# Kernel tuning notes

Measured on AMD Instinct MI355X. Metric: run time of the kernel, lower is better.

The kernel has to match this reference:

```python
import jax, jax.numpy as jnp
import numpy as np

B, N, M = 256, 512, 512


def setup_inputs() -> dict:
    key = jax.random.key(0)
    kx, kw, kt = jax.random.split(key, 3)
    x = jax.random.uniform(kx, (B, N), dtype=jnp.float32)
    w = jax.random.uniform(kw, (N, M), dtype=jnp.float32)
    t = jax.random.uniform(kt, (B, M), dtype=jnp.float32)
    return {"x": x, "w": w, "t": t}


def reference(x, w, t):
    # x: [B, N], w: [N, M], t: [B, M]
    x3 = x[:, :, None]   # [B, N, 1]
    t3 = t[:, None, :]   # [B, 1, M]
    w3 = w[None, :, :]   # [1, N, M]

    # relevance of x per (n, m): sum over batch of min(x, t) / sum over batch of x
    rel_x = jnp.minimum(x3, t3).sum(axis=0, keepdims=True) / x3.sum(axis=0, keepdims=True)  # [1, N, M]
    # relevance of w per (b, m): sum over N of min(w, t) / sum over N of w
    rel_w = jnp.minimum(w3, t3).sum(axis=-2, keepdims=True) / w3.sum(axis=-2, keepdims=True)  # [B, 1, M]

    # argmax over the N (inner) dimension
    ind_w = jnp.argmax(jnp.minimum(x3, rel_x), axis=-2)  # [B, M]
    ind_x = jnp.argmax(jnp.minimum(rel_w, w3), axis=-2)  # [B, M]

    # inner_x and inner_w are numerically identical in forward (detach only affects grads)
    inner = jnp.minimum(x3, w3)  # [B, N, M]
    chosen_x = jnp.take_along_axis(inner, ind_x[:, None, :], axis=-2)[:, 0, :]  # [B, M]
    chosen_w = jnp.take_along_axis(inner, ind_w[:, None, :], axis=-2)[:, 0, :]  # [B, M]
    return (chosen_x, chosen_w)
```

## Files before the change

kernel.cpp:

```cpp
#include <hip/hip_runtime.h>

#define B 256
#define N 512
#define M 512
#define BM (B * M)


__device__ __forceinline__ void tile_tr256(const float* __restrict__ src,
                                           float* __restrict__ dst,
                                           int R, int C, int r0, int c0, int tid) {
    __shared__ float s[64][65];
    const int tx = tid & 63, q = tid >> 6;
    #pragma unroll
    for (int j = 0; j < 16; ++j) {
        int rl = q * 16 + j;
        s[rl][tx] = src[(r0 + rl) * C + c0 + tx];
    }
    __syncthreads();
    #pragma unroll
    for (int j = 0; j < 16; ++j) {
        int cl = q * 16 + j;
        dst[(c0 + cl) * R + r0 + tx] = s[tx][cl];
    }
}

__global__ __launch_bounds__(256) void k_a(const float* __restrict__ x,
                                           const float* __restrict__ w,
                                           const float* __restrict__ t,
                                           float* __restrict__ xT,
                                           float* __restrict__ wT,
                                           float* __restrict__ tT,
                                           float* __restrict__ rvp) {
    const int blk = blockIdx.x, tid = threadIdx.x;
    if (blk < 128) {
        const int m0 = (blk & 7) * 64;
        const int n0 = (blk >> 3) * 32;
        const int tx = tid & 15, ty = tid >> 4;
        __shared__ float  s_t[32][64];
        __shared__ float  s_x[32][36];
        __shared__ double sxc4[32][4];
        const int sr = tid >> 3, sc = tid & 7;
        const int nA = ty * 2, nB = nA + 1;
        float pA0, pA1, pA2, pA3, pB0, pB1, pB2, pB3;
        #pragma unroll
        for (int z = 0; z < 4; ++z) {
            float aA0 = 0.f, aA1 = 0.f, aA2 = 0.f, aA3 = 0.f;
            float aB0 = 0.f, aB1 = 0.f, aB2 = 0.f, aB3 = 0.f;
            for (int scnk = 0; scnk < 2; ++scnk) {
                const int bb = z * 64 + scnk * 32;
                __syncthreads();
                *(float4*)&s_t[sr][sc * 8]     = *(const float4*)&t[(bb + sr) * M + m0 + sc * 8];
                *(float4*)&s_t[sr][sc * 8 + 4] = *(const float4*)&t[(bb + sr) * M + m0 + sc * 8 + 4];
                *(float4*)&s_x[sr][sc * 4]     = *(const float4*)&x[(bb + sr) * N + n0 + sc * 4];
                __syncthreads();
                #pragma unroll 8
                for (int i = 0; i < 32; ++i) {
                    float4 tv = *(const float4*)&s_t[i][tx * 4];
                    float xA = s_x[i][nA], xB = s_x[i][nB];
                    aA0 += fminf(xA, tv.x); aA1 += fminf(xA, tv.y);
                    aA2 += fminf(xA, tv.z); aA3 += fminf(xA, tv.w);
                    aB0 += fminf(xB, tv.x); aB1 += fminf(xB, tv.y);
                    aB2 += fminf(xB, tv.z); aB3 += fminf(xB, tv.w);
                }
            }
            if (z == 0) {
                pA0 = aA0; pA1 = aA1; pA2 = aA2; pA3 = aA3;
                pB0 = aB0; pB1 = aB1; pB2 = aB2; pB3 = aB3;
            } else {
                pA0 += aA0; pA1 += aA1; pA2 += aA2; pA3 += aA3;
                pB0 += aB0; pB1 += aB1; pB2 += aB2; pB3 += aB3;
            }
        }
        if (tid < 128) {
            const int col = n0 + (tid >> 2), ch = tid & 3;
            double a = 0.0;
            for (int b = ch; b < B; b += 4) a += (double)x[b * N + col];
            sxc4[tid >> 2][ch] = a;
        }
        __syncthreads();
        const float sA = (float)((sxc4[nA][0] + sxc4[nA][1]) + (sxc4[nA][2] + sxc4[nA][3]));
        const float sB = (float)((sxc4[nB][0] + sxc4[nB][1]) + (sxc4[nB][2] + sxc4[nB][3]));
        float* so = &s_t[0][0];
        so[(tx * 4 + 0) * 32 + nA] = pA0 / sA; so[(tx * 4 + 0) * 32 + nB] = pB0 / sB;
        so[(tx * 4 + 1) * 32 + nA] = pA1 / sA; so[(tx * 4 + 1) * 32 + nB] = pB1 / sB;
        so[(tx * 4 + 2) * 32 + nA] = pA2 / sA; so[(tx * 4 + 2) * 32 + nB] = pB2 / sB;
        so[(tx * 4 + 3) * 32 + nA] = pA3 / sA; so[(tx * 4 + 3) * 32 + nB] = pB3 / sB;
        __syncthreads();
        const int m_l = tid >> 2, n_l = (tid & 3) * 8;
        float* dst = &rvp[(m0 + m_l) * N + n0 + n_l];
        *(float4*)&dst[0] = *(const float4*)&so[m_l * 32 + n_l];
        *(float4*)&dst[4] = *(const float4*)&so[m_l * 32 + n_l + 4];
    } else if (blk < 160) {
        const int id = blk - 128;
        tile_tr256(x, xT, B, N, (id >> 3) * 64, (id & 7) * 64, tid);
    } else if (blk < 224) {
        const int id = blk - 160;
        tile_tr256(w, wT, N, M, (id >> 3) * 64, (id & 7) * 64, tid);
    } else {
        const int id = blk - 224;
        tile_tr256(t, tT, B, M, (id >> 3) * 64, (id & 7) * 64, tid);
    }
}

__global__ __launch_bounds__(512) void k_col(
        const float* __restrict__ x, const float* __restrict__ xT,
        const float* __restrict__ wT, const float* __restrict__ tT,
        const float* __restrict__ rvp, float* __restrict__ out) {
    const int m = blockIdx.x, tid = threadIdx.x;
    const int lane = tid & 63, wid = tid >> 6;

    __shared__ float  worig[512], pm[512], wsrt[512];
    __shared__ float  srx_r[512], srx_u[512];
    __shared__ int    srx_n[512];
    __shared__ int    cnt[256], cbase[256], cslot[256];
    __shared__ int    rcnt[256], rbase[256], rslot[256], rbmax[256];
    __shared__ double bsumI[256];
    __shared__ double swpart[4];
    __shared__ float  wtotmax[8], red3[3][8];
    __shared__ int    ctot[4], rtot[4];
    __shared__ double btot[4];

    const float wv = wT[m * N + tid];
    const float rv = rvp[m * N + tid];
    worig[tid] = wv;
    if (tid < 256) { cnt[tid] = 0; rcnt[tid] = 0; cslot[tid] = 0; rslot[tid] = 0; rbmax[tid] = 0; }

    float pmv = wv;
    #pragma unroll
    for (int off = 1; off < 64; off <<= 1) {
        float o = __shfl_up(pmv, off, 64);
        if (lane >= off) pmv = fmaxf(pmv, o);
    }
    if (lane == 63) wtotmax[wid] = pmv;
    float wmn = wv, rmn = rv, rmx = rv;
    #pragma unroll
    for (int off = 32; off > 0; off >>= 1) {
        wmn = fminf(wmn, __shfl_xor(wmn, off, 64));
        rmn = fminf(rmn, __shfl_xor(rmn, off, 64));
        rmx = fmaxf(rmx, __shfl_xor(rmx, off, 64));
    }
    if (lane == 0) { red3[0][wid] = wmn; red3[1][wid] = rmn; red3[2][wid] = rmx; }
    __syncthreads();

    if (tid < 4) {
        double a = 0.0;
        for (int n = tid; n < 512; n += 4) a += (double)worig[n];
        swpart[tid] = a;
    }

    {
        float om = -1e30f;
        for (int j = 0; j < wid; ++j) om = fmaxf(om, wtotmax[j]);
        pm[tid] = fmaxf(pmv, om);
    }
    float wmin = red3[0][0], rmin = red3[1][0], rmax = red3[2][0], wmax = wtotmax[0];
    #pragma unroll
    for (int j = 1; j < 8; ++j) {
        wmin = fminf(wmin, red3[0][j]);
        rmin = fminf(rmin, red3[1][j]);
        rmax = fmaxf(rmax, red3[2][j]);
        wmax = fmaxf(wmax, wtotmax[j]);
    }

    const float wscale = 255.0f / fmaxf(wmax - wmin, 1e-30f);
    int wk = (int)((wv - wmin) * wscale);
    wk = wk < 0 ? 0 : (wk > 255 ? 255 : wk);
    atomicAdd(&cnt[wk], 1);
    const float rscale = 255.0f / fmaxf(rmax - rmin, 1e-30f);
    int rk;
    { int kv = (int)((rv - rmin) * rscale); kv = kv < 0 ? 0 : (kv > 255 ? 255 : kv); rk = 255 - kv; }
    atomicAdd(&rcnt[rk], 1);
    atomicMax(&rbmax[rk], __float_as_int(rv));
    __syncthreads();

    int myc = (tid < 256) ? cnt[tid] : rcnt[tid - 256];
    int incl = myc;
    #pragma unroll
    for (int off = 1; off < 64; off <<= 1) {
        int o = __shfl_up(incl, off, 64);
        if (lane >= off) incl += o;
    }
    if (lane == 63) { if (wid < 4) ctot[wid] = incl; else rtot[wid - 4] = incl; }
    __syncthreads();
    if (tid < 256) {
        int eo = 0;
        for (int j = 0; j < wid; ++j) eo += ctot[j];
        cbase[tid] = eo + incl - myc;
    } else {
        int eo = 0, w2 = wid - 4;
        for (int j = 0; j < w2; ++j) eo += rtot[j];
        rbase[tid - 256] = eo + incl - myc;
    }
    __syncthreads();

    { int p1 = cbase[wk] + atomicAdd(&cslot[wk], 1); wsrt[p1] = wv; }
    { int p2 = rbase[rk] + atomicAdd(&rslot[rk], 1);
      srx_r[p2] = rv; srx_n[p2] = tid; srx_u[p2] = __int_as_float(rbmax[rk]); }
    __syncthreads();

    double bincl = 0.0, mysum = 0.0;
    if (tid < 256) {
        int st = cbase[tid], e = st + cnt[tid];
        for (int i = st; i < e; ++i) mysum += (double)wsrt[i];
        bincl = mysum;
        #pragma unroll
        for (int off = 1; off < 64; off <<= 1) {
            double o = __shfl_up(bincl, off, 64);
            if (lane >= off) bincl += o;
        }
        if (lane == 63) btot[wid] = bincl;
    }
    __syncthreads();
    if (tid < 256) {
        double eo = 0.0;
        for (int j = 0; j < wid; ++j) eo += btot[j];
        bsumI[tid] = eo + bincl;
    }
    __syncthreads();

    if (tid < 256) {
        const int b = tid;
        float bv = -1.0f; int bi = 0;
        for (int i = 0; i < 512; ++i) {
            float u = srx_u[i];
            if (__ballot(u >= bv) == 0ULL) break;
            float r = srx_r[i];
            int   n = srx_n[i];
            float xv = xT[n * B + b];
            float v = fminf(xv, r);
            if (v > bv || (v == bv && n < bi)) { bv = v; bi = n; }
        }
        out[BM + b * M + m] = fminf(x[b * N + bi], worig[bi]);
    } else {
        const int b = tid - 256;
        const float tbm = tT[m * B + b];
        float btf = (tbm - wmin) * wscale;
        int kk; double S;
        if (btf < 0.0f) { kk = 0; S = 0.0; }
        else {
            int bt = (int)btf; bt = bt > 255 ? 255 : bt;
            kk = cbase[bt];
            S = (bt > 0) ? bsumI[bt - 1] : 0.0;
            int e = cbase[bt] + cnt[bt];
            for (int i = cbase[bt]; i < e; ++i) {
                float v = wsrt[i];
                if (v < tbm) { ++kk; S += (double)v; }
            }
        }
        double rw = S + (double)tbm * (double)(512 - kk);
        const float sw = (float)((swpart[0] + swpart[1]) + (swpart[2] + swpart[3]));
        float c = (float)rw / sw;
        float tgt = fminf(c, pm[511]);
        int lo = 0, hi = 511;
        while (lo < hi) { int mid = (lo + hi) >> 1; if (pm[mid] >= tgt) hi = mid; else lo = mid + 1; }
        const int ind = lo;
        out[b * M + m] = fminf(x[b * N + ind], worig[ind]);
    }
}

extern "C" void kernel_launch(void* const* d_in, const int* in_sizes, int n_in,
                              void* d_out, int out_size, void* d_ws, size_t ws_size,
                              hipStream_t stream) {
    const float* x = (const float*)d_in[0];
    const float* w = (const float*)d_in[1];
    const float* t = (const float*)d_in[2];
    float* out = (float*)d_out;

    float* ws = (float*)d_ws;
    float* xT  = ws;
    float* wT  = ws + 131072;
    float* tT  = ws + 393216;
    float* rvp = ws + 524288;

    k_a  <<<256, 256, 0, stream>>>(x, w, t, xT, wT, tT, rvp);
    k_col<<<512, 512, 0, stream>>>(x, xT, wT, tT, rvp, out);
}
```

Before: 105.5 us.

## Split rel_x reduction across batch quarters with smaller tiles and more blocks

Result: faster. 93.31 us (-11.6%).

```diff
diff --git a/kernel.cpp b/kernel.cpp
--- a/kernel.cpp
+++ b/kernel.cpp
@@ -8,8 +8,9 @@
 
 __device__ __forceinline__ void tile_tr256(const float* __restrict__ src,
                                            float* __restrict__ dst,
-                                           int R, int C, int r0, int c0, int tid) {
-    __shared__ float s[64][65];
+                                           int R, int C, int r0, int c0,
+                                           int tid, char* smem) {
+    float (*s)[65] = reinterpret_cast<float (*)[65]>(smem);
     const int tx = tid & 63, q = tid >> 6;
     #pragma unroll
     for (int j = 0; j < 16; ++j) {
@@ -23,6 +24,8 @@
         dst[(c0 + cl) * R + r0 + tx] = s[tx][cl];
     }
 }
+
+#define SMEM_BYTES 31232
 
 __global__ __launch_bounds__(256) void k_a(const float* __restrict__ x,
                                            const float* __restrict__ w,
@@ -31,74 +34,81 @@
                                            float* __restrict__ wT,
                                            float* __restrict__ tT,
                                            float* __restrict__ rvp) {
+    __shared__ __align__(16) char smem[SMEM_BYTES];
     const int blk = blockIdx.x, tid = threadIdx.x;
-    if (blk < 128) {
-        const int m0 = (blk & 7) * 64;
-        const int n0 = (blk >> 3) * 32;
-        const int tx = tid & 15, ty = tid >> 4;
-        __shared__ float  s_t[32][64];
-        __shared__ float  s_x[32][36];
-        __shared__ double sxc4[32][4];
-        const int sr = tid >> 3, sc = tid & 7;
-        const int nA = ty * 2, nB = nA + 1;
-        float pA0, pA1, pA2, pA3, pB0, pB1, pB2, pB3;
-        #pragma unroll
-        for (int z = 0; z < 4; ++z) {
-            float aA0 = 0.f, aA1 = 0.f, aA2 = 0.f, aA3 = 0.f;
-            float aB0 = 0.f, aB1 = 0.f, aB2 = 0.f, aB3 = 0.f;
-            for (int scnk = 0; scnk < 2; ++scnk) {
-                const int bb = z * 64 + scnk * 32;
-                __syncthreads();
-                *(float4*)&s_t[sr][sc * 8]     = *(const float4*)&t[(bb + sr) * M + m0 + sc * 8];
-                *(float4*)&s_t[sr][sc * 8 + 4] = *(const float4*)&t[(bb + sr) * M + m0 + sc * 8 + 4];
-                *(float4*)&s_x[sr][sc * 4]     = *(const float4*)&x[(bb + sr) * N + n0 + sc * 4];
-                __syncthreads();
-                #pragma unroll 8
-                for (int i = 0; i < 32; ++i) {
-                    float4 tv = *(const float4*)&s_t[i][tx * 4];
-                    float xA = s_x[i][nA], xB = s_x[i][nB];
-                    aA0 += fminf(xA, tv.x); aA1 += fminf(xA, tv.y);
-                    aA2 += fminf(xA, tv.z); aA3 += fminf(xA, tv.w);
-                    aB0 += fminf(xB, tv.x); aB1 += fminf(xB, tv.y);
-                    aB2 += fminf(xB, tv.z); aB3 += fminf(xB, tv.w);
-                }
-            }
-            if (z == 0) {
-                pA0 = aA0; pA1 = aA1; pA2 = aA2; pA3 = aA3;
-                pB0 = aB0; pB1 = aB1; pB2 = aB2; pB3 = aB3;
-            } else {
-                pA0 += aA0; pA1 += aA1; pA2 += aA2; pA3 += aA3;
-                pB0 += aB0; pB1 += aB1; pB2 += aB2; pB3 += aB3;
-            }
-        }
-        if (tid < 128) {
+    if (blk < 32) {
+        tile_tr256(x, xT, B, N, (blk >> 3) * 64, (blk & 7) * 64, tid, smem);
+    } else if (blk < 96) {
+        const int id = blk - 32;
+        tile_tr256(w, wT, N, M, (id >> 3) * 64, (id & 7) * 64, tid, smem);
+    } else if (blk < 128) {
+        const int id = blk - 96;
+        tile_tr256(t, tT, B, M, (id >> 3) * 64, (id & 7) * 64, tid, smem);
+    } else {
+        const int rb = blk - 128;
+        const int m0 = (rb & 15) * 32;
+        const int n0 = (rb >> 4) * 16;
+        float  (*S_T)[32][40] = reinterpret_cast<float (*)[32][40]>(smem);
+        float  (*S_X)[32][20] = reinterpret_cast<float (*)[32][20]>(smem + 20480);
+        float  (*PZ)[32][17]  = reinterpret_cast<float (*)[32][17]>(smem + 20480);
+        double (*SX4)[4]      = reinterpret_cast<double (*)[4]>(smem + 30720);
+        const int zg = tid >> 6, tl = tid & 63;
+        const int tx = tl & 7, ny = tl >> 3;
+        const int nA = ny * 2, nB = nA + 1;
+        float aA0 = 0.f, aA1 = 0.f, aA2 = 0.f, aA3 = 0.f;
+        float aB0 = 0.f, aB1 = 0.f, aB2 = 0.f, aB3 = 0.f;
+        for (int s = 0; s < 2; ++s) {
+            __syncthreads();
+            #pragma unroll
+            for (int k = 0; k < 4; ++k) {
+                const int f = k * 256 + tid;
+                const int row = f >> 3, c = f & 7;
+                const int z = row >> 5, r = row & 31;
+                *(float4*)&S_T[z][r][c * 4] =
+                    *(const float4*)&t[(z * 64 + s * 32 + r) * M + m0 + c * 4];
+            }
+            #pragma unroll
+            for (int k = 0; k < 2; ++k) {
+                const int f = k * 256 + tid;
+                const int row = f >> 2, c = f & 3;
+                const int z = row >> 5, r = row & 31;
+                *(float4*)&S_X[z][r][c * 4] =
+                    *(const float4*)&x[(z * 64 + s * 32 + r) * N + n0 + c * 4];
+            }
+            __syncthreads();
+            #pragma unroll 8
+            for (int i = 0; i < 32; ++i) {
+                float4 tv = *(const float4*)&S_T[zg][i][tx * 4];
+                float xA = S_X[zg][i][nA], xB = S_X[zg][i][nB];
+                aA0 += fminf(xA, tv.x); aA1 += fminf(xA, tv.y);
+                aA2 += fminf(xA, tv.z); aA3 += fminf(xA, tv.w);
+                aB0 += fminf(xB, tv.x); aB1 += fminf(xB, tv.y);
+                aB2 += fminf(xB, tv.z); aB3 += fminf(xB, tv.w);
+            }
+        }
+        __syncthreads();
+        PZ[zg][tx * 4 + 0][nA] = aA0; PZ[zg][tx * 4 + 0][nB] = aB0;
+        PZ[zg][tx * 4 + 1][nA] = aA1; PZ[zg][tx * 4 + 1][nB] = aB1;
+        PZ[zg][tx * 4 + 2][nA] = aA2; PZ[zg][tx * 4 + 2][nB] = aB2;
+        PZ[zg][tx * 4 + 3][nA] = aA3; PZ[zg][tx * 4 + 3][nB] = aB3;
+        if (tid < 64) {
             const int col = n0 + (tid >> 2), ch = tid & 3;
             double a = 0.0;
             for (int b = ch; b < B; b += 4) a += (double)x[b * N + col];
-            sxc4[tid >> 2][ch] = a;
+            SX4[tid >> 2][ch] = a;
         }
         __syncthreads();
-        const float sA = (float)((sxc4[nA][0] + sxc4[nA][1]) + (sxc4[nA][2] + sxc4[nA][3]));
-        const float sB = (float)((sxc4[nB][0] + sxc4[nB][1]) + (sxc4[nB][2] + sxc4[nB][3]));
-        float* so = &s_t[0][0];
-        so[(tx * 4 + 0) * 32 + nA] = pA0 / sA; so[(tx * 4 + 0) * 32 + nB] = pB0 / sB;
-        so[(tx * 4 + 1) * 32 + nA] = pA1 / sA; so[(tx * 4 + 1) * 32 + nB] = pB1 / sB;
-        so[(tx * 4 + 2) * 32 + nA] = pA2 / sA; so[(tx * 4 + 2) * 32 + nB] = pB2 / sB;
-        so[(tx * 4 + 3) * 32 + nA] = pA3 / sA; so[(tx * 4 + 3) * 32 + nB] = pB3 / sB;
-        __syncthreads();
-        const int m_l = tid >> 2, n_l = (tid & 3) * 8;
-        float* dst = &rvp[(m0 + m_l) * N + n0 + n_l];
-        *(float4*)&dst[0] = *(const float4*)&so[m_l * 32 + n_l];
-        *(float4*)&dst[4] = *(const float4*)&so[m_l * 32 + n_l + 4];
-    } else if (blk < 160) {
-        const int id = blk - 128;
-        tile_tr256(x, xT, B, N, (id >> 3) * 64, (id & 7) * 64, tid);
-    } else if (blk < 224) {
-        const int id = blk - 160;
-        tile_tr256(w, wT, N, M, (id >> 3) * 64, (id & 7) * 64, tid);
-    } else {
-        const int id = blk - 224;
-        tile_tr256(t, tT, B, M, (id >> 3) * 64, (id & 7) * 64, tid);
+        {
+            const int m_l = tid >> 3, np = (tid & 7) * 2;
+            float p0 = PZ[0][m_l][np];
+            p0 += PZ[1][m_l][np]; p0 += PZ[2][m_l][np]; p0 += PZ[3][m_l][np];
+            float p1 = PZ[0][m_l][np + 1];
+            p1 += PZ[1][m_l][np + 1]; p1 += PZ[2][m_l][np + 1]; p1 += PZ[3][m_l][np + 1];
+            const float s0 = (float)((SX4[np][0] + SX4[np][1]) + (SX4[np][2] + SX4[np][3]));
+            const float s1 = (float)((SX4[np + 1][0] + SX4[np + 1][1]) + (SX4[np + 1][2] + SX4[np + 1][3]));
+            float2 rv2; rv2.x = p0 / s0; rv2.y = p1 / s1;
+            *(float2*)&rvp[(m0 + m_l) * N + n0 + np] = rv2;
+        }
     }
 }
 
@@ -272,6 +282,6 @@
     float* tT  = ws + 393216;
     float* rvp = ws + 524288;
 
-    k_a  <<<256, 256, 0, stream>>>(x, w, t, xT, wT, tT, rvp);
+    k_a  <<<640, 256, 0, stream>>>(x, w, t, xT, wT, tT, rvp);
     k_col<<<512, 512, 0, stream>>>(x, xT, wT, tT, rvp, out);
 }
```
